# Performance work log

Hardware: AMD Instinct MI355X
Metric: run time of the kernel (lower is better)

The kernel has to match this reference:

```python
import jax, jax.numpy as jnp
import numpy as np

B, C, W, H, N = 8, 128, 48, 48, 8192


def setup_inputs() -> dict:
    key = jax.random.key(0)
    ks = jax.random.split(key, 16)
    s = 1.0 / np.sqrt(C)
    inp = {
        "feat0": jax.random.normal(ks[0], (B, C, W, H), jnp.float32),
        "feat1": jax.random.normal(ks[1], (B, C, N), jnp.float32),
        "geo_embed": jax.random.normal(ks[2], (B, W * H, C), jnp.float32),
        # Linear weights stored as [in, out]; biases [out].
        "Wq": jax.random.normal(ks[3], (C, C), jnp.float32) * s,
        "bq": jnp.zeros((C,), jnp.float32),
        "Wk": jax.random.normal(ks[4], (C, C), jnp.float32) * s,
        "bk": jnp.zeros((C,), jnp.float32),
        "Wv": jax.random.normal(ks[5], (C, C), jnp.float32) * s,
        "bv": jnp.zeros((C,), jnp.float32),
        "Wo": jax.random.normal(ks[6], (C, C), jnp.float32) * s,
        "bo": jnp.zeros((C,), jnp.float32),
        "Wg": jax.random.normal(ks[7], (C, C), jnp.float32) * s,
        "bg": jnp.zeros((C,), jnp.float32),
        "Wgate": jax.random.normal(ks[8], (2 * C, 1), jnp.float32) * (1.0 / np.sqrt(2 * C)),
        "bgate": jnp.zeros((1,), jnp.float32),
    }
    return inp


def reference(feat0, feat1, geo_embed, Wq, bq, Wk, bk, Wv, bv, Wo, bo, Wg, bg, Wgate, bgate):
    b, c, w, h = feat0.shape
    # b c w h -> b (w h) c
    q_in = feat0.reshape(b, c, w * h).transpose(0, 2, 1)
    pq = q_in @ Wq + bq  # [b, wh, c]

    geo = geo_embed @ Wg + bg  # [b, wh, c]
    gate = jax.nn.sigmoid(jnp.concatenate([pq, geo], axis=-1) @ Wgate + bgate)  # [b, wh, 1]
    pq = pq + gate * geo

    kv_in = feat1.transpose(0, 2, 1)  # [b, n, c]
    pk = kv_in @ Wk + bk
    pv = kv_in @ Wv + bv

    energy = jnp.einsum('bqc,bnc->bqn', pq, pk)  # [b, wh, n]
    # NOTE: original scales AFTER softmax (non-standard, faithful):
    attention = jax.nn.softmax(energy, axis=-1) / jnp.sqrt(jnp.asarray(c, energy.dtype))
    out = jnp.einsum('bqn,bnc->bqc', attention, pv) @ Wo + bo  # [b, wh, c]
    out = out.transpose(0, 2, 1).reshape(b, c, w, h)

    geo_r = geo.transpose(0, 2, 1).reshape(b, c, w, h)
    out = out * (1.0 + jax.nn.sigmoid(geo_r))
    out = out + feat0
    return out
```

## Files before the change

kernel.cpp:

```cpp
#include <hip/hip_runtime.h>

#define B_ 8
#define C_ 128
#define WH_ 2304
#define N_ 8192

typedef unsigned short u16;
typedef float f32x4 __attribute__((ext_vector_type(4)));
typedef short s16x8 __attribute__((ext_vector_type(8)));
typedef short s16x4 __attribute__((ext_vector_type(4)));
typedef unsigned int u32x2 __attribute__((ext_vector_type(2)));

typedef const unsigned int __attribute__((address_space(1))) ga_u32;
typedef unsigned int __attribute__((address_space(3))) lds_u32;

#define LOG2E 1.4426950408889634f
#define MOFF  64.0f

__device__ __forceinline__ float bf2f(u16 u){
    union { unsigned int i; float f; } x; x.i = ((unsigned int)u) << 16; return x.f;
}
__device__ __forceinline__ u16 f2bf(float f){
    union { float f; unsigned int i; } x; x.f = f;
    unsigned int r = x.i + 0x7fffu + ((x.i >> 16) & 1u);
    return (u16)(r >> 16);
}
__device__ __forceinline__ unsigned int cvtpk(float a, float b){
    unsigned int r;
    asm("v_cvt_pk_bf16_f32 %0, %1, %2" : "=v"(r) : "v"(a), "v"(b));
    return r;
}
__device__ __forceinline__ int swz(int row, int col){
    return row*128 + ((((col >> 3) ^ (row & 15)) << 3) | (col & 7));
}
__device__ __forceinline__ f32x4 fzero(){ f32x4 z = {0.f, 0.f, 0.f, 0.f}; return z; }
__device__ __forceinline__ f32x4 fmoff(){ f32x4 z = {-MOFF, -MOFF, -MOFF, -MOFF}; return z; }
__device__ __forceinline__ f32x4 mfma16(s16x8 a, s16x8 b, f32x4 c){
    return __builtin_amdgcn_mfma_f32_16x16x32_bf16(a, b, c, 0, 0, 0);
}
__device__ __forceinline__ void gld16(const void* g, void* l){
    __builtin_amdgcn_global_load_lds((ga_u32*)g, (lds_u32*)l, 16, 0, 0);
}
__device__ __forceinline__ s16x8 ldsf(const u16* p){ return *(const s16x8*)p; }
__device__ __forceinline__ s16x8 cvt8(const float* p){
    s16x8 r;
    #pragma unroll
    for (int j = 0; j < 8; j++) r[j] = (short)f2bf(p[j]);
    return r;
}

__global__ __launch_bounds__(256) void k_prep(
    const float* __restrict__ Wq, const float* __restrict__ Wk,
    const float* __restrict__ Wv, const float* __restrict__ Wo,
    const float* __restrict__ Wg, u16* __restrict__ Wt)
{
    const int gid = blockIdx.x*256 + threadIdx.x;
    const int mi = gid >> 14, e = gid & 16383;
    const int o = e >> 7, i = e & 127;
    const float* src = (mi==0)?Wq:(mi==1)?Wk:(mi==2)?Wv:(mi==3)?Wo:Wg;
    Wt[mi*16384 + o*128 + i] = f2bf(src[i*128 + o]);
}

__global__ __launch_bounds__(512, 4) void k_proj_kv(
    const float* __restrict__ feat1,
    const float* __restrict__ bk, const float* __restrict__ bv,
    const u16* __restrict__ Wt,
    u16* __restrict__ Kb, u16* __restrict__ Vb)
{
    __shared__ __attribute__((aligned(16))) u16 Af[128*128];
    const int t = threadIdx.x;
    const int b = blockIdx.x >> 6;
    const int n0 = (blockIdx.x & 63) * 128;
    for (int idx = t; idx < 128*32; idx += 512){
        const int nl = (idx & 31) << 2, c = idx >> 5;
        const f32x4 v = *(const f32x4*)&feat1[((size_t)b*C_ + c)*N_ + n0 + nl];
        Af[swz(nl+0, c)] = f2bf(v[0]); Af[swz(nl+1, c)] = f2bf(v[1]);
        Af[swz(nl+2, c)] = f2bf(v[2]); Af[swz(nl+3, c)] = f2bf(v[3]);
    }
    __syncthreads();
    const int lane = t & 63, w = t >> 6, qq = lane >> 4, m = lane & 15;
    const int ar = w*16 + m;
    s16x8 aA[4];
    #pragma unroll
    for (int kt = 0; kt < 4; kt++)
        aA[kt] = ldsf(&Af[ar*128 + (((kt*4 + qq) ^ (ar & 15)) << 3)]);
    const u16* WkT = Wt + 16384;
    const u16* WvT = Wt + 32768;
    f32x4 acc[8];
    #pragma unroll
    for (int ct = 0; ct < 8; ct++) acc[ct] = fzero();
    #pragma unroll
    for (int kt = 0; kt < 4; kt++){
        #pragma unroll
        for (int ct = 0; ct < 8; ct++){
            const s16x8 bf = *(const s16x8*)&WkT[(ct*16 + m)*128 + kt*32 + qq*8];
            acc[ct] = mfma16(aA[kt], bf, acc[ct]);
        }
    }
    u16* Ko = Af;
    #pragma unroll
    for (int ct = 0; ct < 8; ct++){
        const int col = ct*16 + m;
        const float bkv = bk[col];
        #pragma unroll
        for (int i = 0; i < 4; i++)
            Ko[swz(w*16 + qq*4 + i, col)] = f2bf(acc[ct][i] + bkv);
    }
    #pragma unroll
    for (int j = 0; j < 4; j++){
        const int chunk = j*64 + lane;
        const int row = w*16 + (chunk >> 4);
        const int cb = chunk & 15;
        s16x8 v = ldsf(&Ko[row*128 + ((cb ^ (row & 15)) << 3)]);
        *(s16x8*)&Kb[((size_t)b*N_ + n0 + row)*C_ + cb*8] = v;
    }
    #pragma unroll
    for (int ct = 0; ct < 8; ct++) acc[ct] = fzero();
    #pragma unroll
    for (int kt = 0; kt < 4; kt++){
        #pragma unroll
        for (int ct = 0; ct < 8; ct++){
            const s16x8 bf = *(const s16x8*)&WvT[(ct*16 + m)*128 + kt*32 + qq*8];
            acc[ct] = mfma16(aA[kt], bf, acc[ct]);
        }
    }
    #pragma unroll
    for (int ct = 0; ct < 8; ct++){
        const int col = ct*16 + m;
        const float bvv = bv[col];
        u32x2 pk;
        pk.x = cvtpk(acc[ct][0] + bvv, acc[ct][1] + bvv);
        pk.y = cvtpk(acc[ct][2] + bvv, acc[ct][3] + bvv);
        *(u32x2*)&Vb[((size_t)b*C_ + col)*N_ + n0 + w*16 + qq*4] = pk;
    }
}

__global__ __launch_bounds__(256, 3) void k_proj_qg(
    const float* __restrict__ feat0, const float* __restrict__ geo,
    const float* __restrict__ bq, const float* __restrict__ bg,
    const float* __restrict__ Wgate, const float* __restrict__ bgate,
    const u16* __restrict__ Wt,
    u16* __restrict__ Qb, u16* __restrict__ Gb)
{
    __shared__ __attribute__((aligned(16))) u16 Aq[64*128];
    const int t = threadIdx.x;
    const int b = blockIdx.x / 36;
    const int r0 = (blockIdx.x % 36) * 64;
    for (int idx = t; idx < 64*32; idx += 256){
        const int r = (idx & 15) << 2, c = idx >> 4;
        const f32x4 v = *(const f32x4*)&feat0[((size_t)b*C_ + c)*WH_ + r0 + r];
        Aq[swz(r+0, c)] = f2bf(v[0]); Aq[swz(r+1, c)] = f2bf(v[1]);
        Aq[swz(r+2, c)] = f2bf(v[2]); Aq[swz(r+3, c)] = f2bf(v[3]);
    }
    __syncthreads();
    const int lane = t & 63, w = t >> 6, qq = lane >> 4, m = lane & 15;
    const int ar = w*16 + m;
    s16x8 aQ[4], aG[4];
    #pragma unroll
    for (int kt = 0; kt < 4; kt++){
        aQ[kt] = ldsf(&Aq[ar*128 + (((kt*4 + qq) ^ (ar & 15)) << 3)]);
        aG[kt] = cvt8(&geo[((size_t)b*WH_ + r0 + ar)*C_ + kt*32 + qq*8]);
    }
    f32x4 accq[8], accg[8];
    #pragma unroll
    for (int ct = 0; ct < 8; ct++){ accq[ct] = fzero(); accg[ct] = fzero(); }
    #pragma unroll
    for (int kt = 0; kt < 4; kt++){
        #pragma unroll
        for (int ct = 0; ct < 8; ct++){
            const int bn = ct*16 + m;
            const s16x8 b1 = *(const s16x8*)&Wt[bn*128 + kt*32 + qq*8];
            const s16x8 b2 = *(const s16x8*)&Wt[65536 + bn*128 + kt*32 + qq*8];
            accq[ct] = mfma16(aQ[kt], b1, accq[ct]);
            accg[ct] = mfma16(aG[kt], b2, accg[ct]);
        }
    }
    #pragma unroll
    for (int ct = 0; ct < 8; ct++){
        const int col = ct*16 + m;
        const float bqv = bq[col], bgv = bg[col];
        #pragma unroll
        for (int i = 0; i < 4; i++){ accq[ct][i] += bqv; accg[ct][i] += bgv; }
    }
    float w1v[8], w2v[8];
    #pragma unroll
    for (int ct = 0; ct < 8; ct++){
        const int col = ct*16 + m;
        w1v[ct] = Wgate[col]; w2v[ct] = Wgate[C_ + col];
    }
    const float bg0 = bgate[0];
    float gate[4];
    #pragma unroll
    for (int i = 0; i < 4; i++){
        float p = 0.f;
        #pragma unroll
        for (int ct = 0; ct < 8; ct++)
            p += accq[ct][i] * w1v[ct] + accg[ct][i] * w2v[ct];
        #pragma unroll
        for (int off = 1; off < 16; off <<= 1) p += __shfl_xor(p, off, 64);
        gate[i] = 1.f / (1.f + __expf(-(p + bg0)));
    }
    u16* St = Aq;
    #pragma unroll
    for (int ct = 0; ct < 8; ct++){
        #pragma unroll
        for (int i = 0; i < 4; i++){
            const float pq = accq[ct][i] + gate[i] * accg[ct][i];
            St[swz(w*16 + qq*4 + i, ct*16 + m)] = f2bf(pq * LOG2E);
        }
    }
    #pragma unroll
    for (int j = 0; j < 4; j++){
        const int chunk = j*64 + lane;
        const int row = w*16 + (chunk >> 4);
        const int cb = chunk & 15;
        s16x8 v = ldsf(&St[row*128 + ((cb ^ (row & 15)) << 3)]);
        *(s16x8*)&Qb[((size_t)b*WH_ + r0 + row)*C_ + cb*8] = v;
    }
    #pragma unroll
    for (int ct = 0; ct < 8; ct++){
        #pragma unroll
        for (int i = 0; i < 4; i++)
            St[swz(w*16 + qq*4 + i, ct*16 + m)] = f2bf(accg[ct][i]);
    }
    #pragma unroll
    for (int j = 0; j < 4; j++){
        const int chunk = j*64 + lane;
        const int row = w*16 + (chunk >> 4);
        const int cb = chunk & 15;
        s16x8 v = ldsf(&St[row*128 + ((cb ^ (row & 15)) << 3)]);
        *(s16x8*)&Gb[((size_t)b*WH_ + r0 + row)*C_ + cb*8] = v;
    }
}

__global__ __launch_bounds__(1024, 4) void k_flash(
    const u16* __restrict__ Qb, const u16* __restrict__ Kb, const u16* __restrict__ Vb,
    u16* __restrict__ Opart, float* __restrict__ Lp)
{
    __shared__ __attribute__((aligned(16))) u16 KP0[128*128];
    __shared__ __attribute__((aligned(16))) u16 KP1[128*128];
    __shared__ __attribute__((aligned(16))) u16 Vt0[128*128];
    __shared__ __attribute__((aligned(16))) u16 Vt1[128*128];
    const int t = threadIdx.x;
    const int lane = t & 63, w = t >> 6;
    const int q = lane >> 4, m = lane & 15;
    const int b = blockIdx.x & 7;
    const int s = blockIdx.x >> 3;

    f32x4 o[8];
    f32x4 l_acc;
    s16x8 qf[4];
    s16x8 ones8;
    #pragma unroll
    for (int j = 0; j < 8; j++) ones8[j] = (short)0x3F80;

    auto issue = [&](int k){
        const int u = s*18 + k;
        const int n0 = (u & 63) * 128;
        u16* KPd = (k & 1) ? KP1 : KP0;
        u16* Vtd = (k & 1) ? Vt1 : Vt0;
        #pragma unroll
        for (int j = 0; j < 2; j++){
            const int r = w*8 + j*4 + q;
            const int pr = (r & 96) | ((r & 12) << 1) | ((r & 16) >> 2) | (r & 3);
            gld16(Kb + ((size_t)b*N_ + n0 + pr)*C_ + ((m ^ (r & 15)) << 3), &KPd[(w*8 + j*4)*128]);
            gld16(Vb + ((size_t)b*C_ + r)*N_ + n0 + ((m ^ (r & 15)) << 3), &Vtd[(w*8 + j*4)*128]);
        }
    };
    auto load_q = [&](int qb){
        const size_t qrow0 = (size_t)b*WH_ + qb*256;
        #pragma unroll
        for (int kt = 0; kt < 4; kt++)
            qf[kt] = *(const s16x8*)&Qb[(qrow0 + w*16 + m)*C_ + kt*32 + q*8];
    };
    auto zero_acc = [&](){
        #pragma unroll
        for (int ct = 0; ct < 8; ct++) o[ct] = fzero();
        l_acc = fzero();
    };
    auto flush = [&](int qb){
        const int sf = (qb * 64) / 18;
        const size_t pbase = ((size_t)(b*9 + qb)*5 + (s - sf)) * 256;
        #pragma unroll
        for (int ct = 0; ct < 8; ct++){
            u32x2 pk;
            pk.x = cvtpk(o[ct][0], o[ct][1]);
            pk.y = cvtpk(o[ct][2], o[ct][3]);
            *(u32x2*)&Opart[(pbase + w*16 + m)*128 + ct*16 + q*4] = pk;
        }
        if (q == 0) Lp[pbase + w*16 + m] = l_acc[0];
    };

    issue(0);
    int cur_qb = (s*18) >> 6;
    load_q(cur_qb);
    zero_acc();

    for (int k = 0; k < 18; k++){
        __syncthreads();
        if (k < 17) issue(k + 1);
        const u16* KPc = (k & 1) ? KP1 : KP0;
        const u16* Vtc = (k & 1) ? Vt1 : Vt0;

        #pragma unroll
        for (int h = 0; h < 2; h++){
            s16x4 pexp[4];
            #pragma unroll
            for (int n2 = 0; n2 < 4; n2++){
                const int nt = h*4 + n2;
                f32x4 s0 = fmoff();
                const int bn = nt*16 + m;
                #pragma unroll
                for (int kt = 0; kt < 4; kt++){
                    s16x8 kf = ldsf(&KPc[bn*128 + (((kt*4 + q) ^ (bn & 15)) << 3)]);
                    s0 = mfma16(kf, qf[kt], s0);
                }
                union { u32x2 u; s16x4 v; } pp;
                pp.u.x = cvtpk(exp2f(s0[0]), exp2f(s0[1]));
                pp.u.y = cvtpk(exp2f(s0[2]), exp2f(s0[3]));
                pexp[n2] = pp.v;
            }
            const s16x8 p80 = __builtin_shufflevector(pexp[0], pexp[1], 0,1,2,3,4,5,6,7);
            const s16x8 p81 = __builtin_shufflevector(pexp[2], pexp[3], 0,1,2,3,4,5,6,7);
            l_acc = mfma16(ones8, p80, l_acc);
            l_acc = mfma16(ones8, p81, l_acc);
            #pragma unroll
            for (int ct = 0; ct < 8; ct++){
                const int cc = ct*16 + m;
                const int pair0 = h*2;
                s16x8 vf0 = ldsf(&Vtc[cc*128 + ((((pair0+0)*4 + q) ^ (cc & 15)) << 3)]);
                s16x8 vf1 = ldsf(&Vtc[cc*128 + ((((pair0+1)*4 + q) ^ (cc & 15)) << 3)]);
                o[ct] = mfma16(vf0, p80, o[ct]);
                o[ct] = mfma16(vf1, p81, o[ct]);
            }
        }
        const int nqb = (k < 17) ? ((s*18 + k + 1) >> 6) : -1;
        if (nqb != cur_qb){
            flush(cur_qb);
            if (nqb >= 0){ load_q(nqb); zero_acc(); cur_qb = nqb; }
        }
    }
}

__global__ __launch_bounds__(256) void k_out(
    const u16* __restrict__ Opart, const float* __restrict__ Lp,
    const float* __restrict__ bo, const u16* __restrict__ Wt,
    const u16* __restrict__ Gb, const float* __restrict__ feat0,
    float* __restrict__ outp)
{
    __shared__ __attribute__((aligned(16))) u16 AO[128*128];
    __shared__ u16 Tr[128*130];
    const int t = threadIdx.x;
    const int bqt = blockIdx.x;
    const int qt2 = bqt >> 1, half = bqt & 1;
    const int b = qt2 / 9, qb = qt2 % 9;
    const int gr0 = qb*256 + half*128;
    const u16* WoT = Wt + 49152;
    const float rsC = 0.088388347648318447f;
    const int sf = (qb*64) / 18;
    const int sl = (qb*64 + 63) / 18;
    const int cnt = sl - sf + 1;
    for (int idx = t; idx < 128*16; idx += 256){
        int r = idx >> 4, cb = idx & 15;
        float num[8];
        #pragma unroll
        for (int j = 0; j < 8; j++) num[j] = 0.f;
        float den = 0.f;
        for (int ss = 0; ss < cnt; ss++){
            const size_t base = ((size_t)qt2*5 + ss)*256 + half*128 + r;
            s16x8 v = *(const s16x8*)&Opart[base*128 + cb*8];
            #pragma unroll
            for (int j = 0; j < 8; j++) num[j] += bf2f((u16)v[j]);
            den += Lp[base];
        }
        const float sc = rsC / den;
        s16x8 o8;
        #pragma unroll
        for (int j = 0; j < 8; j++) o8[j] = (short)f2bf(num[j] * sc);
        *(s16x8*)&AO[r*128 + ((cb ^ (r & 15)) << 3)] = o8;
    }
    __syncthreads();
    const int lane = t & 63, w = t >> 6;
    const int q = lane >> 4, m = lane & 15;
    const int rw = w * 32;
    f32x4 acc[2][8];
    #pragma unroll
    for (int rt = 0; rt < 2; rt++){
        #pragma unroll
        for (int ct = 0; ct < 8; ct++) acc[rt][ct] = fzero();
    }
    #pragma unroll
    for (int kt = 0; kt < 4; kt++){
        s16x8 a0, a1;
        { const int ar = rw + m;      a0 = ldsf(&AO[ar*128 + (((kt*4 + q) ^ (ar & 15)) << 3)]); }
        { const int ar = rw + 16 + m; a1 = ldsf(&AO[ar*128 + (((kt*4 + q) ^ (ar & 15)) << 3)]); }
        #pragma unroll
        for (int ct = 0; ct < 8; ct++){
            const s16x8 bb = *(const s16x8*)&WoT[(ct*16 + m)*128 + kt*32 + q*8];
            acc[0][ct] = mfma16(a0, bb, acc[0][ct]);
            acc[1][ct] = mfma16(a1, bb, acc[1][ct]);
        }
    }
    #pragma unroll
    for (int ct = 0; ct < 8; ct++){
        const int col = ct*16 + m;
        const float bov = bo[col];
        #pragma unroll
        for (int rt = 0; rt < 2; rt++){
            #pragma unroll
            for (int i = 0; i < 4; i++){
                const int rl = rw + rt*16 + q*4 + i;
                const float gv = bf2f(Gb[((size_t)b*WH_ + gr0 + rl)*C_ + col]);
                const float sg = 1.f / (1.f + __expf(-gv));
                Tr[rl*130 + col] = f2bf((acc[rt][ct][i] + bov) * (1.f + sg));
            }
        }
    }
    __syncthreads();
    for (int idx = t; idx < 128*128; idx += 256){
        int c = idx >> 7, wh = idx & 127;
        float v = bf2f(Tr[wh*130 + c]) + feat0[(size_t)(b*C_ + c)*WH_ + gr0 + wh];
        outp[(size_t)(b*C_ + c)*WH_ + gr0 + wh] = v;
    }
}

extern "C" void kernel_launch(void* const* d_in, const int* in_sizes, int n_in,
                              void* d_out, int out_size, void* d_ws, size_t ws_size,
                              hipStream_t stream)
{
    (void)in_sizes; (void)n_in; (void)out_size; (void)ws_size;
    const float* feat0 = (const float*)d_in[0];
    const float* feat1 = (const float*)d_in[1];
    const float* geo   = (const float*)d_in[2];
    const float* Wq = (const float*)d_in[3];  const float* bq = (const float*)d_in[4];
    const float* Wk = (const float*)d_in[5];  const float* bk = (const float*)d_in[6];
    const float* Wv = (const float*)d_in[7];  const float* bv = (const float*)d_in[8];
    const float* Wo = (const float*)d_in[9];  const float* bo = (const float*)d_in[10];
    const float* Wg = (const float*)d_in[11]; const float* bg = (const float*)d_in[12];
    const float* Wgate = (const float*)d_in[13]; const float* bgate = (const float*)d_in[14];
    float* outp = (float*)d_out;
    char* ws = (char*)d_ws;
    size_t off = 0;
    auto alloc = [&](size_t bytes) -> void* {
        void* p = (void*)(ws + off);
        off += (bytes + 255) & ~(size_t)255;
        return p;
    };
    u16* Qb = (u16*)alloc((size_t)B_*WH_*C_*2);
    u16* Gb = (u16*)alloc((size_t)B_*WH_*C_*2);
    u16* Kb = (u16*)alloc((size_t)B_*N_*C_*2);
    u16* Vb = (u16*)alloc((size_t)B_*N_*C_*2);
    u16* Opart = (u16*)alloc((size_t)72*5*256*128*2);
    float* Lp  = (float*)alloc((size_t)72*5*256*4);
    u16* Wt = (u16*)alloc((size_t)5*16384*2);

    k_prep   <<<dim3(320), dim3(256), 0, stream>>>(Wq, Wk, Wv, Wo, Wg, Wt);
    k_proj_kv<<<dim3(512), dim3(512), 0, stream>>>(feat1, bk, bv, Wt, Kb, Vb);
    k_proj_qg<<<dim3(288), dim3(256), 0, stream>>>(feat0, geo, bq, bg, Wgate, bgate, Wt, Qb, Gb);
    k_flash  <<<dim3(256), dim3(1024), 0, stream>>>(Qb, Kb, Vb, Opart, Lp);
    k_out    <<<dim3(144), dim3(256), 0, stream>>>(Opart, Lp, bo, Wt, Gb, feat0, outp);
}
```

Before: 286.1 us.

## Merge K/V and Q/G projections into one launch and shrink output tiles

```diff
diff --git a/kernel.cpp b/kernel.cpp
--- a/kernel.cpp
+++ b/kernel.cpp
@@ -61,29 +61,25 @@
     Wt[mi*16384 + o*128 + i] = f2bf(src[i*128 + o]);
 }
 
-__global__ __launch_bounds__(512, 4) void k_proj_kv(
+__device__ __forceinline__ void proj_kv_body(
+    u16* SB, int blk,
     const float* __restrict__ feat1,
     const float* __restrict__ bk, const float* __restrict__ bv,
     const u16* __restrict__ Wt,
     u16* __restrict__ Kb, u16* __restrict__ Vb)
 {
-    __shared__ __attribute__((aligned(16))) u16 Af[128*128];
     const int t = threadIdx.x;
-    const int b = blockIdx.x >> 6;
-    const int n0 = (blockIdx.x & 63) * 128;
-    for (int idx = t; idx < 128*32; idx += 512){
-        const int nl = (idx & 31) << 2, c = idx >> 5;
-        const f32x4 v = *(const f32x4*)&feat1[((size_t)b*C_ + c)*N_ + n0 + nl];
-        Af[swz(nl+0, c)] = f2bf(v[0]); Af[swz(nl+1, c)] = f2bf(v[1]);
-        Af[swz(nl+2, c)] = f2bf(v[2]); Af[swz(nl+3, c)] = f2bf(v[3]);
-    }
-    __syncthreads();
+    const int b = blk >> 7;
+    const int n0 = (blk & 127) * 64;
     const int lane = t & 63, w = t >> 6, qq = lane >> 4, m = lane & 15;
-    const int ar = w*16 + m;
+    const int nr = n0 + w*16 + m;
     s16x8 aA[4];
     #pragma unroll
-    for (int kt = 0; kt < 4; kt++)
-        aA[kt] = ldsf(&Af[ar*128 + (((kt*4 + qq) ^ (ar & 15)) << 3)]);
+    for (int kt = 0; kt < 4; kt++){
+        #pragma unroll
+        for (int j = 0; j < 8; j++)
+            aA[kt][j] = (short)f2bf(feat1[((size_t)b*C_ + kt*32 + qq*8 + j)*N_ + nr]);
+    }
     const u16* WkT = Wt + 16384;
     const u16* WvT = Wt + 32768;
     f32x4 acc[8];
@@ -97,21 +93,20 @@
             acc[ct] = mfma16(aA[kt], bf, acc[ct]);
         }
     }
-    u16* Ko = Af;
     #pragma unroll
     for (int ct = 0; ct < 8; ct++){
         const int col = ct*16 + m;
         const float bkv = bk[col];
         #pragma unroll
         for (int i = 0; i < 4; i++)
-            Ko[swz(w*16 + qq*4 + i, col)] = f2bf(acc[ct][i] + bkv);
+            SB[swz(w*16 + qq*4 + i, col)] = f2bf(acc[ct][i] + bkv);
     }
     #pragma unroll
     for (int j = 0; j < 4; j++){
         const int chunk = j*64 + lane;
         const int row = w*16 + (chunk >> 4);
         const int cb = chunk & 15;
-        s16x8 v = ldsf(&Ko[row*128 + ((cb ^ (row & 15)) << 3)]);
+        s16x8 v = ldsf(&SB[row*128 + ((cb ^ (row & 15)) << 3)]);
         *(s16x8*)&Kb[((size_t)b*N_ + n0 + row)*C_ + cb*8] = v;
     }
     #pragma unroll
@@ -135,30 +130,25 @@
     }
 }
 
-__global__ __launch_bounds__(256, 3) void k_proj_qg(
+__device__ __forceinline__ void proj_qg_body(
+    u16* SB, int blk,
     const float* __restrict__ feat0, const float* __restrict__ geo,
     const float* __restrict__ bq, const float* __restrict__ bg,
     const float* __restrict__ Wgate, const float* __restrict__ bgate,
     const u16* __restrict__ Wt,
     u16* __restrict__ Qb, u16* __restrict__ Gb)
 {
-    __shared__ __attribute__((aligned(16))) u16 Aq[64*128];
     const int t = threadIdx.x;
-    const int b = blockIdx.x / 36;
-    const int r0 = (blockIdx.x % 36) * 64;
-    for (int idx = t; idx < 64*32; idx += 256){
-        const int r = (idx & 15) << 2, c = idx >> 4;
-        const f32x4 v = *(const f32x4*)&feat0[((size_t)b*C_ + c)*WH_ + r0 + r];
-        Aq[swz(r+0, c)] = f2bf(v[0]); Aq[swz(r+1, c)] = f2bf(v[1]);
-        Aq[swz(r+2, c)] = f2bf(v[2]); Aq[swz(r+3, c)] = f2bf(v[3]);
-    }
-    __syncthreads();
+    const int b = blk / 36;
+    const int r0 = (blk % 36) * 64;
     const int lane = t & 63, w = t >> 6, qq = lane >> 4, m = lane & 15;
     const int ar = w*16 + m;
     s16x8 aQ[4], aG[4];
     #pragma unroll
     for (int kt = 0; kt < 4; kt++){
-        aQ[kt] = ldsf(&Aq[ar*128 + (((kt*4 + qq) ^ (ar & 15)) << 3)]);
+        #pragma unroll
+        for (int j = 0; j < 8; j++)
+            aQ[kt][j] = (short)f2bf(feat0[((size_t)b*C_ + kt*32 + qq*8 + j)*WH_ + r0 + ar]);
         aG[kt] = cvt8(&geo[((size_t)b*WH_ + r0 + ar)*C_ + kt*32 + qq*8]);
     }
     f32x4 accq[8], accg[8];
@@ -200,13 +190,12 @@
         for (int off = 1; off < 16; off <<= 1) p += __shfl_xor(p, off, 64);
         gate[i] = 1.f / (1.f + __expf(-(p + bg0)));
     }
-    u16* St = Aq;
     #pragma unroll
     for (int ct = 0; ct < 8; ct++){
         #pragma unroll
         for (int i = 0; i < 4; i++){
             const float pq = accq[ct][i] + gate[i] * accg[ct][i];
-            St[swz(w*16 + qq*4 + i, ct*16 + m)] = f2bf(pq * LOG2E);
+            SB[swz(w*16 + qq*4 + i, ct*16 + m)] = f2bf(pq * LOG2E);
         }
     }
     #pragma unroll
@@ -214,23 +203,40 @@
         const int chunk = j*64 + lane;
         const int row = w*16 + (chunk >> 4);
         const int cb = chunk & 15;
-        s16x8 v = ldsf(&St[row*128 + ((cb ^ (row & 15)) << 3)]);
+        s16x8 v = ldsf(&SB[row*128 + ((cb ^ (row & 15)) << 3)]);
         *(s16x8*)&Qb[((size_t)b*WH_ + r0 + row)*C_ + cb*8] = v;
     }
     #pragma unroll
     for (int ct = 0; ct < 8; ct++){
         #pragma unroll
         for (int i = 0; i < 4; i++)
-            St[swz(w*16 + qq*4 + i, ct*16 + m)] = f2bf(accg[ct][i]);
+            SB[swz(w*16 + qq*4 + i, ct*16 + m)] = f2bf(accg[ct][i]);
     }
     #pragma unroll
     for (int j = 0; j < 4; j++){
         const int chunk = j*64 + lane;
         const int row = w*16 + (chunk >> 4);
         const int cb = chunk & 15;
-        s16x8 v = ldsf(&St[row*128 + ((cb ^ (row & 15)) << 3)]);
+        s16x8 v = ldsf(&SB[row*128 + ((cb ^ (row & 15)) << 3)]);
         *(s16x8*)&Gb[((size_t)b*WH_ + r0 + row)*C_ + cb*8] = v;
     }
+}
+
+__global__ __launch_bounds__(256, 3) void k_proj(
+    const float* __restrict__ feat1,
+    const float* __restrict__ bk, const float* __restrict__ bv,
+    const float* __restrict__ feat0, const float* __restrict__ geo,
+    const float* __restrict__ bq, const float* __restrict__ bg,
+    const float* __restrict__ Wgate, const float* __restrict__ bgate,
+    const u16* __restrict__ Wt,
+    u16* __restrict__ Kb, u16* __restrict__ Vb,
+    u16* __restrict__ Qb, u16* __restrict__ Gb)
+{
+    __shared__ __attribute__((aligned(16))) u16 SB[64*128];
+    if (blockIdx.x < 1024)
+        proj_kv_body(SB, blockIdx.x, feat1, bk, bv, Wt, Kb, Vb);
+    else
+        proj_qg_body(SB, blockIdx.x - 1024, feat0, geo, bq, bg, Wgate, bgate, Wt, Qb, Gb);
 }
 
 __global__ __launch_bounds__(1024, 4) void k_flash(
@@ -342,32 +348,32 @@
     }
 }
 
-__global__ __launch_bounds__(256) void k_out(
+__global__ __launch_bounds__(256, 4) void k_out(
     const u16* __restrict__ Opart, const float* __restrict__ Lp,
     const float* __restrict__ bo, const u16* __restrict__ Wt,
     const u16* __restrict__ Gb, const float* __restrict__ feat0,
     float* __restrict__ outp)
 {
-    __shared__ __attribute__((aligned(16))) u16 AO[128*128];
-    __shared__ u16 Tr[128*130];
+    __shared__ __attribute__((aligned(16))) u16 AO[64*128];
     const int t = threadIdx.x;
-    const int bqt = blockIdx.x;
-    const int qt2 = bqt >> 1, half = bqt & 1;
-    const int b = qt2 / 9, qb = qt2 % 9;
-    const int gr0 = qb*256 + half*128;
+    const int r36 = blockIdx.x % 36;
+    const int b = blockIdx.x / 36;
+    const int qb = r36 >> 2, quarter = r36 & 3;
+    const int gr0 = qb*256 + quarter*64;
+    const int qt2 = b*9 + qb;
     const u16* WoT = Wt + 49152;
     const float rsC = 0.088388347648318447f;
     const int sf = (qb*64) / 18;
     const int sl = (qb*64 + 63) / 18;
     const int cnt = sl - sf + 1;
-    for (int idx = t; idx < 128*16; idx += 256){
+    for (int idx = t; idx < 64*16; idx += 256){
         int r = idx >> 4, cb = idx & 15;
         float num[8];
         #pragma unroll
         for (int j = 0; j < 8; j++) num[j] = 0.f;
         float den = 0.f;
         for (int ss = 0; ss < cnt; ss++){
-            const size_t base = ((size_t)qt2*5 + ss)*256 + half*128 + r;
+            const size_t base = ((size_t)qt2*5 + ss)*256 + quarter*64 + r;
             s16x8 v = *(const s16x8*)&Opart[base*128 + cb*8];
             #pragma unroll
             for (int j = 0; j < 8; j++) num[j] += bf2f((u16)v[j]);
@@ -382,44 +388,36 @@
     __syncthreads();
     const int lane = t & 63, w = t >> 6;
     const int q = lane >> 4, m = lane & 15;
-    const int rw = w * 32;
-    f32x4 acc[2][8];
-    #pragma unroll
-    for (int rt = 0; rt < 2; rt++){
-        #pragma unroll
-        for (int ct = 0; ct < 8; ct++) acc[rt][ct] = fzero();
-    }
-    #pragma unroll
-    for (int kt = 0; kt < 4; kt++){
-        s16x8 a0, a1;
-        { const int ar = rw + m;      a0 = ldsf(&AO[ar*128 + (((kt*4 + q) ^ (ar & 15)) << 3)]); }
-        { const int ar = rw + 16 + m; a1 = ldsf(&AO[ar*128 + (((kt*4 + q) ^ (ar & 15)) << 3)]); }
+    f32x4 acc[8];
+    #pragma unroll
+    for (int ct = 0; ct < 8; ct++) acc[ct] = fzero();
+    #pragma unroll
+    for (int kt = 0; kt < 4; kt++){
+        const int ar = w*16 + m;
+        const s16x8 a0 = ldsf(&AO[ar*128 + (((kt*4 + q) ^ (ar & 15)) << 3)]);
         #pragma unroll
         for (int ct = 0; ct < 8; ct++){
             const s16x8 bb = *(const s16x8*)&WoT[(ct*16 + m)*128 + kt*32 + q*8];
-            acc[0][ct] = mfma16(a0, bb, acc[0][ct]);
-            acc[1][ct] = mfma16(a1, bb, acc[1][ct]);
-        }
-    }
+            acc[ct] = mfma16(a0, bb, acc[ct]);
+        }
+    }
+    u16* Tr = AO;
     #pragma unroll
     for (int ct = 0; ct < 8; ct++){
         const int col = ct*16 + m;
         const float bov = bo[col];
         #pragma unroll
-        for (int rt = 0; rt < 2; rt++){
-            #pragma unroll
-            for (int i = 0; i < 4; i++){
-                const int rl = rw + rt*16 + q*4 + i;
-                const float gv = bf2f(Gb[((size_t)b*WH_ + gr0 + rl)*C_ + col]);
-                const float sg = 1.f / (1.f + __expf(-gv));
-                Tr[rl*130 + col] = f2bf((acc[rt][ct][i] + bov) * (1.f + sg));
-            }
+        for (int i = 0; i < 4; i++){
+            const int rl = w*16 + q*4 + i;
+            const float gv = bf2f(Gb[((size_t)b*WH_ + gr0 + rl)*C_ + col]);
+            const float sg = 1.f / (1.f + __expf(-gv));
+            Tr[swz(rl, col)] = f2bf((acc[ct][i] + bov) * (1.f + sg));
         }
     }
     __syncthreads();
-    for (int idx = t; idx < 128*128; idx += 256){
-        int c = idx >> 7, wh = idx & 127;
-        float v = bf2f(Tr[wh*130 + c]) + feat0[(size_t)(b*C_ + c)*WH_ + gr0 + wh];
+    for (int idx = t; idx < 64*128; idx += 256){
+        int c = idx >> 6, wh = idx & 63;
+        float v = bf2f(Tr[swz(wh, c)]) + feat0[(size_t)(b*C_ + c)*WH_ + gr0 + wh];
         outp[(size_t)(b*C_ + c)*WH_ + gr0 + wh] = v;
     }
 }
@@ -454,9 +452,9 @@
     float* Lp  = (float*)alloc((size_t)72*5*256*4);
     u16* Wt = (u16*)alloc((size_t)5*16384*2);
 
-    k_prep   <<<dim3(320), dim3(256), 0, stream>>>(Wq, Wk, Wv, Wo, Wg, Wt);
-    k_proj_kv<<<dim3(512), dim3(512), 0, stream>>>(feat1, bk, bv, Wt, Kb, Vb);
-    k_proj_qg<<<dim3(288), dim3(256), 0, stream>>>(feat0, geo, bq, bg, Wgate, bgate, Wt, Qb, Gb);
-    k_flash  <<<dim3(256), dim3(1024), 0, stream>>>(Qb, Kb, Vb, Opart, Lp);
-    k_out    <<<dim3(144), dim3(256), 0, stream>>>(Opart, Lp, bo, Wt, Gb, feat0, outp);
-}
+    k_prep <<<dim3(320),  dim3(256),  0, stream>>>(Wq, Wk, Wv, Wo, Wg, Wt);
+    k_proj <<<dim3(1312), dim3(256),  0, stream>>>(feat1, bk, bv, feat0, geo, bq, bg,
+                                                   Wgate, bgate, Wt, Kb, Vb, Qb, Gb);
+    k_flash<<<dim3(256),  dim3(1024), 0, stream>>>(Qb, Kb, Vb, Opart, Lp);
+    k_out  <<<dim3(288),  dim3(256),  0, stream>>>(Opart, Lp, bo, Wt, Gb, feat0, outp);
+}
```

New measurement: 272.4 us (median of 2 runs). 1.05x faster.
